# Kernel tuning notes

Hardware: AMD Instinct MI355X
Metric: run time of the kernel (lower is better)

## Reference

```python
import jax, jax.numpy as jnp
import numpy as np

B, T, D, U = 64, 2048, 256, 256
EPS = 1e-6


def setup_inputs() -> dict:
    key = jax.random.key(0)
    ks = jax.random.split(key, 4)
    x = jax.random.normal(ks[0], (B, T, D), dtype=jnp.float32)
    # glorot-ish scaled init for stability
    kernel = jax.random.normal(ks[1], (D, 3 * U), dtype=jnp.float32) * (1.0 / np.sqrt(D))
    rec_kernel = jax.random.normal(ks[2], (U, 3 * U), dtype=jnp.float32) * (1.0 / np.sqrt(U))
    bias = jnp.zeros((3 * U,), dtype=jnp.float32)
    ln_gamma = jnp.ones((U,), dtype=jnp.float32)
    ln_beta = jnp.zeros((U,), dtype=jnp.float32)
    return {"x": x, "kernel": kernel, "rec_kernel": rec_kernel, "bias": bias,
            "ln_gamma": ln_gamma, "ln_beta": ln_beta}


def _custom_gru(x, kernel, rec_kernel, bias):
    # Precompute input projection for all timesteps: [B,T,3U]
    xw = jnp.einsum('btd,dk->btk', x, kernel) + bias
    xw_t = jnp.swapaxes(xw, 0, 1)  # [T,B,3U] for scan
    h0 = jnp.zeros((x.shape[0], U), dtype=x.dtype)

    def step(h, xw_step):
        gates = xw_step + h @ rec_kernel            # [B,3U]
        z, r, h_hat_pre = jnp.split(gates, 3, axis=1)
        z = jax.nn.sigmoid(z)
        r = jax.nn.sigmoid(r)
        # nonstandard blend inside tanh (faithful to CustomGRUCell)
        h_hat = jnp.tanh(r * h_hat_pre + (1.0 - r) * h)
        h_new = (1.0 - z) * h_hat + z * h
        return h_new, h_new

    _, hs = jax.lax.scan(step, h0, xw_t)            # hs: [T,B,U]
    return jnp.swapaxes(hs, 0, 1)                   # [B,T,U]


def _layernorm(x, gamma, beta):
    mu = jnp.mean(x, axis=-1, keepdims=True)
    var = jnp.mean(jnp.square(x - mu), axis=-1, keepdims=True)
    return (x - mu) * jax.lax.rsqrt(var + EPS) * gamma + beta


def reference(x, kernel, rec_kernel, bias, ln_gamma, ln_beta):
    # call() returns only the GRU-stack branch (n=1 layer) + shared LayerNorm;
    # the embedded_inputs branch in the source is dead code.
    seq = _custom_gru(x, kernel, rec_kernel, bias)
    return _layernorm(seq, ln_gamma, ln_beta)
```

## Files before the change

### kernel.cpp

```cpp
#include <hip/hip_runtime.h>
#include <hip/hip_bf16.h>
#include <hip/hip_fp16.h>

using half4_t = __attribute__((ext_vector_type(4))) _Float16;
using half8_t = __attribute__((ext_vector_type(8))) _Float16;
using f32x4   = __attribute__((ext_vector_type(4))) float;
using i32x4   = __attribute__((ext_vector_type(4))) int;

#define B_   64
#define T_   2048
#define D_   256
#define U_   256
#define NG   768
#define TC   512
#define NCHUNK (T_/TC)
#define GB   16

typedef const __attribute__((address_space(1))) void* gptr_t;
typedef __attribute__((address_space(3))) void* lptr_t;

__device__ __forceinline__ float rcpf(float x) { return __builtin_amdgcn_rcpf(x); }


__global__ void conv_x_chunk(const float* __restrict__ x, _Float16* __restrict__ xh, int t0) {
  size_t idx = ((size_t)blockIdx.x * 256 + threadIdx.x) * 8;
  int b   = (int)(idx >> 17);
  int rem = (int)(idx & 131071);
  const float4* p = (const float4*)(x + ((size_t)(b * T_ + t0)) * D_ + rem);
  float4 v0 = p[0], v1 = p[1];
  half8_t o;
  o[0] = (_Float16)v0.x; o[1] = (_Float16)v0.y; o[2] = (_Float16)v0.z; o[3] = (_Float16)v0.w;
  o[4] = (_Float16)v1.x; o[5] = (_Float16)v1.y; o[6] = (_Float16)v1.z; o[7] = (_Float16)v1.w;
  *(half8_t*)(xh + idx) = o;
}

__global__ void conv_T(const float* __restrict__ src, _Float16* __restrict__ dst) {
  int idx = blockIdx.x * 256 + threadIdx.x;
  int d = idx / NG;
  int j = idx - d * NG;
  dst[j * 256 + d] = (_Float16)src[idx];
}


__global__ void init_scale(unsigned* s) { if (threadIdx.x == 0) *s = 0u; }

__global__ void absmax_rec(const float* __restrict__ rec, unsigned* __restrict__ s) {
  int i = (blockIdx.x * 256 + threadIdx.x) * 4;
  float4 v = *(const float4*)(rec + i);
  float m = fmaxf(fmaxf(fabsf(v.x), fabsf(v.y)), fmaxf(fabsf(v.z), fabsf(v.w)));
  #pragma unroll
  for (int off = 32; off >= 1; off >>= 1) m = fmaxf(m, __shfl_xor(m, off));
  __shared__ float sm[4];
  int l = threadIdx.x & 63, wv = threadIdx.x >> 6;
  if (l == 0) sm[wv] = m;
  __syncthreads();
  if (threadIdx.x == 0) {
    m = fmaxf(fmaxf(sm[0], sm[1]), fmaxf(sm[2], sm[3]));
    atomicMax(s, __float_as_uint(m));
  }
}

__global__ void conv_rec_i8(const float* __restrict__ rec, const unsigned* __restrict__ sc,
                            char* __restrict__ dst) {
  int idx = blockIdx.x * 256 + threadIdx.x;
  int j = idx & 15, l = (idx >> 4) & 63, sl = idx >> 10;
  int mt = sl >> 2, ks = sl & 3, bi = l & 15, hi = l >> 4;
  float am = __uint_as_float(*sc) + 1e-30f;
  float s = 127.f / am;
  float v = rec[(size_t)(ks * 64 + hi * 16 + j) * NG + mt * 16 + bi] * s;
  int q = __float2int_rn(v);
  q = q > 127 ? 127 : (q < -127 ? -127 : q);
  dst[idx] = (char)q;
}

#define BM 128
#define BN 128

__global__ __launch_bounds__(256, 2) void gemm16(
    const _Float16* __restrict__ A,
    const _Float16* __restrict__ BT,
    const float* __restrict__ bias,
    _Float16* __restrict__ xwl)
{
  __shared__ alignas(16) _Float16 As[BM * 32];
  __shared__ alignas(16) _Float16 Bs[BN * 32];
  const int tid = threadIdx.x, l = tid & 63, w = tid >> 6;
  const int NT = NG / BN;
  const int mt = blockIdx.x / NT, nt = blockIdx.x % NT;
  const char* Ab = (const char*)A  + (size_t)mt * BM * 512;
  const char* Bb = (const char*)BT + (size_t)nt * BN * 512;
  const int wm = (w & 1) * 64, wn = (w >> 1) * 64;
  f32x4 acc[4][4] = {};

  for (int kt = 0; kt < 8; ++kt) {
    #pragma unroll
    for (int s = 0; s < 2; ++s) {
      int c = tid + s * 256;
      int row = c >> 2, gq = c & 3;
      int gs = gq ^ ((row >> 1) & 3);
      __builtin_amdgcn_global_load_lds(
        (gptr_t)(Ab + (size_t)row * 512 + kt * 64 + gs * 16),
        (lptr_t)((char*)As + c * 16), 16, 0, 0);
    }
    #pragma unroll
    for (int s = 0; s < 2; ++s) {
      int c = tid + s * 256;
      int row = c >> 2, gq = c & 3;
      int gs = gq ^ ((row >> 1) & 3);
      __builtin_amdgcn_global_load_lds(
        (gptr_t)(Bb + (size_t)row * 512 + kt * 64 + gs * 16),
        (lptr_t)((char*)Bs + c * 16), 16, 0, 0);
    }
    __syncthreads();

    half8_t av[4], bv[4];
    #pragma unroll
    for (int m = 0; m < 4; ++m) {
      int row = wm + m * 16 + (l & 15);
      int off = row * 64 + (((l >> 4) ^ ((row >> 1) & 3)) << 4);
      av[m] = *(const half8_t*)((const char*)As + off);
    }
    #pragma unroll
    for (int n = 0; n < 4; ++n) {
      int row = wn + n * 16 + (l & 15);
      int off = row * 64 + (((l >> 4) ^ ((row >> 1) & 3)) << 4);
      bv[n] = *(const half8_t*)((const char*)Bs + off);
    }
    #pragma unroll
    for (int m = 0; m < 4; ++m)
      #pragma unroll
      for (int n = 0; n < 4; ++n)
        acc[m][n] = __builtin_amdgcn_mfma_f32_16x16x32_f16(av[m], bv[n], acc[m][n], 0, 0, 0);
    __syncthreads();
  }

  int m0 = mt * BM, n0 = nt * BN;
  #pragma unroll
  for (int m = 0; m < 4; ++m) {
    #pragma unroll
    for (int n = 0; n < 4; ++n) {
      int c = n0 + wn + n * 16 + (l & 15);
      int gate = c >> 8, uu = c & 255;
      int wv = uu >> 4, hq = (uu >> 2) & 3, qv = uu & 3;
      int lane_tid = wv * 64 + (qv << 2) + (hq << 4);
      float bc = bias[c];
      #pragma unroll
      for (int q = 0; q < 4; ++q) {
        int arow = m0 + wm + m * 16 + ((l >> 4) * 4 + q);
        int b = arow >> 9, tloc = arow & 511;
        int g = b >> 2, bidx = b & 3;
        size_t dst = ((size_t)(g * 512 + tloc) * 3 + gate) * 1024 + lane_tid + bidx;
        xwl[dst] = (_Float16)(acc[m][n][q] + bc);
      }
    }
  }
}


__global__ __launch_bounds__(1024) void scan_i8(
    const char* __restrict__ rq,
    const _Float16* __restrict__ xws,
    const unsigned* __restrict__ sc,
    float* __restrict__ out,
    float* __restrict__ hg,
    int t0)
{
  const int g = blockIdx.x, tid = threadIdx.x;
  const int w = tid >> 6, l = tid & 63, bi = l & 15, hi = l >> 4;
  const int bc = bi & 3, qq = bi >> 2;
  const int u = w * 16 + hi * 4 + qq;

  __shared__ alignas(16) char Hq[2][1024];

  const i32x4* rp = (const i32x4*)rq;
#define FR(mt, ks) rp[((mt) * 4 + (ks)) * 64 + l]
  i32x4 Az0 = FR(w, 0),      Az1 = FR(w, 1),      Az2 = FR(w, 2),      Az3 = FR(w, 3);
  i32x4 Ar0 = FR(16 + w, 0), Ar1 = FR(16 + w, 1), Ar2 = FR(16 + w, 2), Ar3 = FR(16 + w, 3);
  i32x4 Ah0 = FR(32 + w, 0), Ah1 = FR(32 + w, 1), Ah2 = FR(32 + w, 2), Ah3 = FR(32 + w, 3);
#undef FR
  asm volatile("" : "+v"(Az0), "+v"(Az1), "+v"(Az2), "+v"(Az3),
                    "+v"(Ar0), "+v"(Ar1), "+v"(Ar2), "+v"(Ar3),
                    "+v"(Ah0), "+v"(Ah1), "+v"(Ah2), "+v"(Ah3));

  const float dq = (__uint_as_float(*sc) + 1e-30f) / (127.f * 127.f);

  float h = (t0 == 0) ? 0.f : hg[(size_t)(g * 4 + bc) * 256 + u];

  const int hwa = bc * 256 + ((w ^ bc) << 4) + hi * 4 + qq;
  { int q8 = __float2int_rn(h * 127.f); Hq[0][hwa] = (char)q8; }

  const _Float16* xp = xws + (size_t)g * 512 * 3072 + tid;
  float* outp = out + ((size_t)(g * 4 + bc) * T_ + t0) * U_ + u;

  _Float16 nz = xp[0], nr = xp[1024], nh = xp[2048];
  __syncthreads();

  for (int t = 0; t < TC; ++t) {
    float xzf = (float)nz, xrf = (float)nr, xhf = (float)nh;
    {
      int tn = (t + 1 < TC) ? (t + 1) : t;
      const _Float16* xq = xp + (size_t)tn * 3072;
      nz = xq[0]; nr = xq[1024]; nh = xq[2048];
    }

    const char* hb = &Hq[t & 1][0];
    i32x4 az = {}, ar = {}, ah = {};
#define BADDR(ks) (bc * 256 + ((((ks) * 4 + hi) ^ bc) << 4))
    { i32x4 Bf;
      Bf = *(const i32x4*)(hb + BADDR(0));
      az = __builtin_amdgcn_mfma_i32_16x16x64_i8(Az0, Bf, az, 0, 0, 0);
      ar = __builtin_amdgcn_mfma_i32_16x16x64_i8(Ar0, Bf, ar, 0, 0, 0);
      ah = __builtin_amdgcn_mfma_i32_16x16x64_i8(Ah0, Bf, ah, 0, 0, 0);
      Bf = *(const i32x4*)(hb + BADDR(1));
      az = __builtin_amdgcn_mfma_i32_16x16x64_i8(Az1, Bf, az, 0, 0, 0);
      ar = __builtin_amdgcn_mfma_i32_16x16x64_i8(Ar1, Bf, ar, 0, 0, 0);
      ah = __builtin_amdgcn_mfma_i32_16x16x64_i8(Ah1, Bf, ah, 0, 0, 0);
      Bf = *(const i32x4*)(hb + BADDR(2));
      az = __builtin_amdgcn_mfma_i32_16x16x64_i8(Az2, Bf, az, 0, 0, 0);
      ar = __builtin_amdgcn_mfma_i32_16x16x64_i8(Ar2, Bf, ar, 0, 0, 0);
      ah = __builtin_amdgcn_mfma_i32_16x16x64_i8(Ah2, Bf, ah, 0, 0, 0);
      Bf = *(const i32x4*)(hb + BADDR(3));
      az = __builtin_amdgcn_mfma_i32_16x16x64_i8(Az3, Bf, az, 0, 0, 0);
      ar = __builtin_amdgcn_mfma_i32_16x16x64_i8(Ar3, Bf, ar, 0, 0, 0);
      ah = __builtin_amdgcn_mfma_i32_16x16x64_i8(Ah3, Bf, ah, 0, 0, 0);
    }
#undef BADDR

#define SEL4(a) ((qq & 2) ? ((qq & 1) ? (a)[3] : (a)[2]) : ((qq & 1) ? (a)[1] : (a)[0]))
    float pz = (float)SEL4(az) * dq + xzf;
    float pr = (float)SEL4(ar) * dq + xrf;
    float ph = (float)SEL4(ah) * dq + xhf;
#undef SEL4
    float z  = rcpf(1.f + __expf(-pz));
    float r  = rcpf(1.f + __expf(-pr));
    float y  = r * (ph - h) + h;
    float th = 2.f * rcpf(1.f + __expf(-2.f * y)) - 1.f;
    h = z * (h - th) + th;

    outp[(size_t)t * U_] = h;
    int q8 = __float2int_rn(h * 127.f);
    Hq[(t & 1) ^ 1][hwa] = (char)q8;
    __syncthreads();
  }

  hg[(size_t)(g * 4 + bc) * 256 + u] = h;
}

__global__ __launch_bounds__(256) void ln_rows(
    float* __restrict__ io,
    const float* __restrict__ gamma, const float* __restrict__ beta, int t0)
{
  int rid = blockIdx.x * 4 + (threadIdx.x >> 6);
  int l = threadIdx.x & 63;
  int b = rid >> 9, tl = rid & 511;
  float* p = io + ((size_t)b * T_ + t0 + tl) * U_ + l * 4;
  f32x4 v = *(const f32x4*)p;
  float s  = (v[0] + v[1]) + (v[2] + v[3]);
  float s2 = (v[0]*v[0] + v[1]*v[1]) + (v[2]*v[2] + v[3]*v[3]);
  #pragma unroll
  for (int off = 1; off <= 32; off <<= 1) {
    s  += __shfl_xor(s, off);
    s2 += __shfl_xor(s2, off);
  }
  float mu = s * (1.f / 256.f);
  float var = s2 * (1.f / 256.f) - mu * mu;
  float rs = rsqrtf(var + 1e-6f);
  f32x4 gm = *(const f32x4*)(gamma + l * 4);
  f32x4 bt = *(const f32x4*)(beta + l * 4);
  f32x4 o;
  o[0] = (v[0] - mu) * rs * gm[0] + bt[0];
  o[1] = (v[1] - mu) * rs * gm[1] + bt[1];
  o[2] = (v[2] - mu) * rs * gm[2] + bt[2];
  o[3] = (v[3] - mu) * rs * gm[3] + bt[3];
  *(f32x4*)p = o;
}

extern "C" void kernel_launch(void* const* d_in, const int* in_sizes, int n_in,
                              void* d_out, int out_size, void* d_ws, size_t ws_size,
                              hipStream_t stream) {
  const float* x     = (const float*)d_in[0];
  const float* kern  = (const float*)d_in[1];
  const float* rec   = (const float*)d_in[2];
  const float* bias  = (const float*)d_in[3];
  const float* gamma = (const float*)d_in[4];
  const float* beta  = (const float*)d_in[5];
  float* out = (float*)d_out;
  char* ws = (char*)d_ws;

  _Float16* xws = (_Float16*)(ws);
  _Float16* xhc = (_Float16*)(ws + 50331648);
  _Float16* kT  = (_Float16*)(ws + 67108864);
  char*     rq  = (char*)    (ws + 67502080);
  unsigned* sc  = (unsigned*)(ws + 67698688);
  float*    hg  = (float*)   (ws + 67698720);

  init_scale<<<1, 64, 0, stream>>>(sc);
  absmax_rec<<<192, 256, 0, stream>>>(rec, sc);
  conv_T<<<768, 256, 0, stream>>>(kern, kT);
  conv_rec_i8<<<768, 256, 0, stream>>>(rec, sc, rq);

  for (int c = 0; c < NCHUNK; ++c) {
    int t0 = c * TC;
    conv_x_chunk<<<4096, 256, 0, stream>>>(x, xhc, t0);
    gemm16<<<(B_ * TC / BM) * (NG / BN), 256, 0, stream>>>(xhc, kT, bias, xws);
    scan_i8<<<GB, 1024, 0, stream>>>(rq, xws, sc, out, hg, t0);
    ln_rows<<<(B_ * TC) / 4, 256, 0, stream>>>(out, gamma, beta, t0);
  }
}
```

Before: 1.581 ms.

## Fuse scan, GEMM and LayerNorm into one kernel and pipeline chunks

Replaces the separate gemm16, scan_i8 and ln_rows kernels with one 'mega' kernel that dispatches on block index to scan, GEMM-tile or LayerNorm work. The host schedule is software-pipelined over time chunks: the 16 latency-bound scan blocks for chunk c run alongside the GEMM for chunk c+1 and the LayerNorm for chunk c-1, using double-buffered projection buffers. This aims to hide input-projection and normalization time behind the sequential recurrence and to fill idle CUs. The projection layout now interleaves z and r gates as half2, so the scan loads them in one access. Risks: the pipelined path only runs when the workspace is large enough, and co-running blocks may contend with the scan for memory bandwidth.

```diff
diff --git a/kernel.cpp b/kernel.cpp
--- a/kernel.cpp
+++ b/kernel.cpp
@@ -2,7 +2,7 @@
 #include <hip/hip_bf16.h>
 #include <hip/hip_fp16.h>
 
-using half4_t = __attribute__((ext_vector_type(4))) _Float16;
+using half2_t = __attribute__((ext_vector_type(2))) _Float16;
 using half8_t = __attribute__((ext_vector_type(8))) _Float16;
 using f32x4   = __attribute__((ext_vector_type(4))) float;
 using i32x4   = __attribute__((ext_vector_type(4))) int;
@@ -14,7 +14,9 @@
 #define NG   768
 #define TC   512
 #define NCHUNK (T_/TC)
-#define GB   16
+#define GB_SCAN 16
+#define GB_GEMM 1536
+#define GB_LN   2048
 
 typedef const __attribute__((address_space(1))) void* gptr_t;
 typedef __attribute__((address_space(3))) void* lptr_t;
@@ -40,7 +42,6 @@
   int j = idx - d * NG;
   dst[j * 256 + d] = (_Float16)src[idx];
 }
-
 
 __global__ void init_scale(unsigned* s) { if (threadIdx.x == 0) *s = 0u; }
 
@@ -73,206 +74,209 @@
   dst[idx] = (char)q;
 }
 
-#define BM 128
-#define BN 128
-
-__global__ __launch_bounds__(256, 2) void gemm16(
-    const _Float16* __restrict__ A,
-    const _Float16* __restrict__ BT,
-    const float* __restrict__ bias,
-    _Float16* __restrict__ xwl)
-{
-  __shared__ alignas(16) _Float16 As[BM * 32];
-  __shared__ alignas(16) _Float16 Bs[BN * 32];
-  const int tid = threadIdx.x, l = tid & 63, w = tid >> 6;
-  const int NT = NG / BN;
-  const int mt = blockIdx.x / NT, nt = blockIdx.x % NT;
-  const char* Ab = (const char*)A  + (size_t)mt * BM * 512;
-  const char* Bb = (const char*)BT + (size_t)nt * BN * 512;
-  const int wm = (w & 1) * 64, wn = (w >> 1) * 64;
-  f32x4 acc[4][4] = {};
-
-  for (int kt = 0; kt < 8; ++kt) {
-    #pragma unroll
-    for (int s = 0; s < 2; ++s) {
-      int c = tid + s * 256;
-      int row = c >> 2, gq = c & 3;
-      int gs = gq ^ ((row >> 1) & 3);
-      __builtin_amdgcn_global_load_lds(
-        (gptr_t)(Ab + (size_t)row * 512 + kt * 64 + gs * 16),
-        (lptr_t)((char*)As + c * 16), 16, 0, 0);
-    }
-    #pragma unroll
-    for (int s = 0; s < 2; ++s) {
-      int c = tid + s * 256;
-      int row = c >> 2, gq = c & 3;
-      int gs = gq ^ ((row >> 1) & 3);
-      __builtin_amdgcn_global_load_lds(
-        (gptr_t)(Bb + (size_t)row * 512 + kt * 64 + gs * 16),
-        (lptr_t)((char*)Bs + c * 16), 16, 0, 0);
-    }
-    __syncthreads();
-
-    half8_t av[4], bv[4];
-    #pragma unroll
-    for (int m = 0; m < 4; ++m) {
-      int row = wm + m * 16 + (l & 15);
-      int off = row * 64 + (((l >> 4) ^ ((row >> 1) & 3)) << 4);
-      av[m] = *(const half8_t*)((const char*)As + off);
-    }
-    #pragma unroll
-    for (int n = 0; n < 4; ++n) {
-      int row = wn + n * 16 + (l & 15);
-      int off = row * 64 + (((l >> 4) ^ ((row >> 1) & 3)) << 4);
-      bv[n] = *(const half8_t*)((const char*)Bs + off);
-    }
-    #pragma unroll
-    for (int m = 0; m < 4; ++m)
-      #pragma unroll
-      for (int n = 0; n < 4; ++n)
-        acc[m][n] = __builtin_amdgcn_mfma_f32_16x16x32_f16(av[m], bv[n], acc[m][n], 0, 0, 0);
-    __syncthreads();
-  }
-
-  int m0 = mt * BM, n0 = nt * BN;
-  #pragma unroll
-  for (int m = 0; m < 4; ++m) {
-    #pragma unroll
-    for (int n = 0; n < 4; ++n) {
-      int c = n0 + wn + n * 16 + (l & 15);
-      int gate = c >> 8, uu = c & 255;
-      int wv = uu >> 4, hq = (uu >> 2) & 3, qv = uu & 3;
-      int lane_tid = wv * 64 + (qv << 2) + (hq << 4);
-      float bc = bias[c];
-      #pragma unroll
-      for (int q = 0; q < 4; ++q) {
-        int arow = m0 + wm + m * 16 + ((l >> 4) * 4 + q);
-        int b = arow >> 9, tloc = arow & 511;
-        int g = b >> 2, bidx = b & 3;
-        size_t dst = ((size_t)(g * 512 + tloc) * 3 + gate) * 1024 + lane_tid + bidx;
-        xwl[dst] = (_Float16)(acc[m][n][q] + bc);
-      }
-    }
-  }
-}
-
-
-__global__ __launch_bounds__(1024) void scan_i8(
+
+__global__ __launch_bounds__(1024) void mega(
     const char* __restrict__ rq,
-    const _Float16* __restrict__ xws,
+    const _Float16* __restrict__ xwsS,
     const unsigned* __restrict__ sc,
     float* __restrict__ out,
     float* __restrict__ hg,
-    int t0)
+    int scanT0,
+    const _Float16* __restrict__ xhc,
+    const _Float16* __restrict__ kT,
+    const float* __restrict__ bias,
+    _Float16* __restrict__ xwsG,
+    const float* __restrict__ gamma,
+    const float* __restrict__ beta,
+    int lnT0,
+    int nScan, int nGemm)
 {
-  const int g = blockIdx.x, tid = threadIdx.x;
-  const int w = tid >> 6, l = tid & 63, bi = l & 15, hi = l >> 4;
-  const int bc = bi & 3, qq = bi >> 2;
-  const int u = w * 16 + hi * 4 + qq;
-
-  __shared__ alignas(16) char Hq[2][1024];
-
-  const i32x4* rp = (const i32x4*)rq;
+  __shared__ union UU {
+    struct { char Hq[2][1024]; } s;
+    struct { alignas(16) _Float16 As[128 * 32]; alignas(16) _Float16 Bs[128 * 32]; } g;
+  } U;
+
+  int bid = blockIdx.x;
+  const int tid = threadIdx.x;
+
+  if (bid < nScan) {
+    const int g = bid;
+    const int w = tid >> 6, l = tid & 63, bi = l & 15, hi = l >> 4;
+    const int bc = bi & 3, qq = bi >> 2;
+    const int u = w * 16 + hi * 4 + qq;
+
+    const i32x4* rp = (const i32x4*)rq;
 #define FR(mt, ks) rp[((mt) * 4 + (ks)) * 64 + l]
-  i32x4 Az0 = FR(w, 0),      Az1 = FR(w, 1),      Az2 = FR(w, 2),      Az3 = FR(w, 3);
-  i32x4 Ar0 = FR(16 + w, 0), Ar1 = FR(16 + w, 1), Ar2 = FR(16 + w, 2), Ar3 = FR(16 + w, 3);
-  i32x4 Ah0 = FR(32 + w, 0), Ah1 = FR(32 + w, 1), Ah2 = FR(32 + w, 2), Ah3 = FR(32 + w, 3);
+    i32x4 Az0 = FR(w, 0),      Az1 = FR(w, 1),      Az2 = FR(w, 2),      Az3 = FR(w, 3);
+    i32x4 Ar0 = FR(16 + w, 0), Ar1 = FR(16 + w, 1), Ar2 = FR(16 + w, 2), Ar3 = FR(16 + w, 3);
+    i32x4 Ah0 = FR(32 + w, 0), Ah1 = FR(32 + w, 1), Ah2 = FR(32 + w, 2), Ah3 = FR(32 + w, 3);
 #undef FR
-  asm volatile("" : "+v"(Az0), "+v"(Az1), "+v"(Az2), "+v"(Az3),
-                    "+v"(Ar0), "+v"(Ar1), "+v"(Ar2), "+v"(Ar3),
-                    "+v"(Ah0), "+v"(Ah1), "+v"(Ah2), "+v"(Ah3));
-
-  const float dq = (__uint_as_float(*sc) + 1e-30f) / (127.f * 127.f);
-
-  float h = (t0 == 0) ? 0.f : hg[(size_t)(g * 4 + bc) * 256 + u];
-
-  const int hwa = bc * 256 + ((w ^ bc) << 4) + hi * 4 + qq;
-  { int q8 = __float2int_rn(h * 127.f); Hq[0][hwa] = (char)q8; }
-
-  const _Float16* xp = xws + (size_t)g * 512 * 3072 + tid;
-  float* outp = out + ((size_t)(g * 4 + bc) * T_ + t0) * U_ + u;
-
-  _Float16 nz = xp[0], nr = xp[1024], nh = xp[2048];
-  __syncthreads();
-
-  for (int t = 0; t < TC; ++t) {
-    float xzf = (float)nz, xrf = (float)nr, xhf = (float)nh;
-    {
-      int tn = (t + 1 < TC) ? (t + 1) : t;
-      const _Float16* xq = xp + (size_t)tn * 3072;
-      nz = xq[0]; nr = xq[1024]; nh = xq[2048];
-    }
-
-    const char* hb = &Hq[t & 1][0];
-    i32x4 az = {}, ar = {}, ah = {};
+    asm volatile("" : "+v"(Az0), "+v"(Az1), "+v"(Az2), "+v"(Az3),
+                      "+v"(Ar0), "+v"(Ar1), "+v"(Ar2), "+v"(Ar3),
+                      "+v"(Ah0), "+v"(Ah1), "+v"(Ah2), "+v"(Ah3));
+
+    const float dq = (__uint_as_float(*sc) + 1e-30f) / (127.f * 127.f);
+
+    float h = (scanT0 == 0) ? 0.f : hg[(size_t)(g * 4 + bc) * 256 + u];
+
+    const int hwa = bc * 256 + ((w ^ bc) << 4) + hi * 4 + qq;
+    { int q8 = __float2int_rn(h * 127.f); U.s.Hq[0][hwa] = (char)q8; }
+
+    const char* xpg = (const char*)xwsS + (size_t)g * TC * 6144;
+    float* outp = out + ((size_t)(g * 4 + bc) * T_ + scanT0) * U_ + u;
+
+    unsigned nzr = *(const unsigned*)(xpg + tid * 4);
+    _Float16 nh2 = *(const _Float16*)(xpg + 4096 + tid * 2);
+    __syncthreads();
+
+    for (int t = 0; t < TC; ++t) {
+      half2_t zrp = __builtin_bit_cast(half2_t, nzr);
+      float xzf = (float)zrp[0], xrf = (float)zrp[1], xhf = (float)nh2;
+      {
+        int tn = (t + 1 < TC) ? (t + 1) : t;
+        nzr = *(const unsigned*)(xpg + (size_t)tn * 6144 + tid * 4);
+        nh2 = *(const _Float16*)(xpg + (size_t)tn * 6144 + 4096 + tid * 2);
+      }
+
+      const char* hb = &U.s.Hq[t & 1][0];
+      i32x4 az = {}, ar = {}, ah = {};
 #define BADDR(ks) (bc * 256 + ((((ks) * 4 + hi) ^ bc) << 4))
-    { i32x4 Bf;
-      Bf = *(const i32x4*)(hb + BADDR(0));
-      az = __builtin_amdgcn_mfma_i32_16x16x64_i8(Az0, Bf, az, 0, 0, 0);
-      ar = __builtin_amdgcn_mfma_i32_16x16x64_i8(Ar0, Bf, ar, 0, 0, 0);
-      ah = __builtin_amdgcn_mfma_i32_16x16x64_i8(Ah0, Bf, ah, 0, 0, 0);
-      Bf = *(const i32x4*)(hb + BADDR(1));
-      az = __builtin_amdgcn_mfma_i32_16x16x64_i8(Az1, Bf, az, 0, 0, 0);
-      ar = __builtin_amdgcn_mfma_i32_16x16x64_i8(Ar1, Bf, ar, 0, 0, 0);
-      ah = __builtin_amdgcn_mfma_i32_16x16x64_i8(Ah1, Bf, ah, 0, 0, 0);
-      Bf = *(const i32x4*)(hb + BADDR(2));
-      az = __builtin_amdgcn_mfma_i32_16x16x64_i8(Az2, Bf, az, 0, 0, 0);
-      ar = __builtin_amdgcn_mfma_i32_16x16x64_i8(Ar2, Bf, ar, 0, 0, 0);
-      ah = __builtin_amdgcn_mfma_i32_16x16x64_i8(Ah2, Bf, ah, 0, 0, 0);
-      Bf = *(const i32x4*)(hb + BADDR(3));
-      az = __builtin_amdgcn_mfma_i32_16x16x64_i8(Az3, Bf, az, 0, 0, 0);
-      ar = __builtin_amdgcn_mfma_i32_16x16x64_i8(Ar3, Bf, ar, 0, 0, 0);
-      ah = __builtin_amdgcn_mfma_i32_16x16x64_i8(Ah3, Bf, ah, 0, 0, 0);
-    }
+      { i32x4 Bf;
+        Bf = *(const i32x4*)(hb + BADDR(0));
+        az = __builtin_amdgcn_mfma_i32_16x16x64_i8(Az0, Bf, az, 0, 0, 0);
+        ar = __builtin_amdgcn_mfma_i32_16x16x64_i8(Ar0, Bf, ar, 0, 0, 0);
+        ah = __builtin_amdgcn_mfma_i32_16x16x64_i8(Ah0, Bf, ah, 0, 0, 0);
+        Bf = *(const i32x4*)(hb + BADDR(1));
+        az = __builtin_amdgcn_mfma_i32_16x16x64_i8(Az1, Bf, az, 0, 0, 0);
+        ar = __builtin_amdgcn_mfma_i32_16x16x64_i8(Ar1, Bf, ar, 0, 0, 0);
+        ah = __builtin_amdgcn_mfma_i32_16x16x64_i8(Ah1, Bf, ah, 0, 0, 0);
+        Bf = *(const i32x4*)(hb + BADDR(2));
+        az = __builtin_amdgcn_mfma_i32_16x16x64_i8(Az2, Bf, az, 0, 0, 0);
+        ar = __builtin_amdgcn_mfma_i32_16x16x64_i8(Ar2, Bf, ar, 0, 0, 0);
+        ah = __builtin_amdgcn_mfma_i32_16x16x64_i8(Ah2, Bf, ah, 0, 0, 0);
+        Bf = *(const i32x4*)(hb + BADDR(3));
+        az = __builtin_amdgcn_mfma_i32_16x16x64_i8(Az3, Bf, az, 0, 0, 0);
+        ar = __builtin_amdgcn_mfma_i32_16x16x64_i8(Ar3, Bf, ar, 0, 0, 0);
+        ah = __builtin_amdgcn_mfma_i32_16x16x64_i8(Ah3, Bf, ah, 0, 0, 0);
+      }
 #undef BADDR
 
 #define SEL4(a) ((qq & 2) ? ((qq & 1) ? (a)[3] : (a)[2]) : ((qq & 1) ? (a)[1] : (a)[0]))
-    float pz = (float)SEL4(az) * dq + xzf;
-    float pr = (float)SEL4(ar) * dq + xrf;
-    float ph = (float)SEL4(ah) * dq + xhf;
+      float pz = (float)SEL4(az) * dq + xzf;
+      float pr = (float)SEL4(ar) * dq + xrf;
+      float ph = (float)SEL4(ah) * dq + xhf;
 #undef SEL4
-    float z  = rcpf(1.f + __expf(-pz));
-    float r  = rcpf(1.f + __expf(-pr));
-    float y  = r * (ph - h) + h;
-    float th = 2.f * rcpf(1.f + __expf(-2.f * y)) - 1.f;
-    h = z * (h - th) + th;
-
-    outp[(size_t)t * U_] = h;
-    int q8 = __float2int_rn(h * 127.f);
-    Hq[(t & 1) ^ 1][hwa] = (char)q8;
-    __syncthreads();
-  }
-
-  hg[(size_t)(g * 4 + bc) * 256 + u] = h;
-}
-
-__global__ __launch_bounds__(256) void ln_rows(
-    float* __restrict__ io,
-    const float* __restrict__ gamma, const float* __restrict__ beta, int t0)
-{
-  int rid = blockIdx.x * 4 + (threadIdx.x >> 6);
-  int l = threadIdx.x & 63;
-  int b = rid >> 9, tl = rid & 511;
-  float* p = io + ((size_t)b * T_ + t0 + tl) * U_ + l * 4;
-  f32x4 v = *(const f32x4*)p;
-  float s  = (v[0] + v[1]) + (v[2] + v[3]);
-  float s2 = (v[0]*v[0] + v[1]*v[1]) + (v[2]*v[2] + v[3]*v[3]);
-  #pragma unroll
-  for (int off = 1; off <= 32; off <<= 1) {
-    s  += __shfl_xor(s, off);
-    s2 += __shfl_xor(s2, off);
-  }
-  float mu = s * (1.f / 256.f);
-  float var = s2 * (1.f / 256.f) - mu * mu;
-  float rs = rsqrtf(var + 1e-6f);
-  f32x4 gm = *(const f32x4*)(gamma + l * 4);
-  f32x4 bt = *(const f32x4*)(beta + l * 4);
-  f32x4 o;
-  o[0] = (v[0] - mu) * rs * gm[0] + bt[0];
-  o[1] = (v[1] - mu) * rs * gm[1] + bt[1];
-  o[2] = (v[2] - mu) * rs * gm[2] + bt[2];
-  o[3] = (v[3] - mu) * rs * gm[3] + bt[3];
-  *(f32x4*)p = o;
+      float z  = rcpf(1.f + __expf(-pz));
+      float r  = rcpf(1.f + __expf(-pr));
+      float y  = r * (ph - h) + h;
+      float th = 2.f * rcpf(1.f + __expf(-2.f * y)) - 1.f;
+      h = z * (h - th) + th;
+
+      outp[(size_t)t * U_] = h;
+      int q8 = __float2int_rn(h * 127.f);
+      U.s.Hq[(t & 1) ^ 1][hwa] = (char)q8;
+      __syncthreads();
+    }
+
+    hg[(size_t)(g * 4 + bc) * 256 + u] = h;
+    return;
+  }
+  bid -= nScan;
+
+  if (bid < nGemm) {
+    const int tile = bid;
+    const int mt = tile / 6, nt = tile % 6;
+    const int w = tid >> 6, l = tid & 63;
+    const int wm = (w & 3) * 32, wn = (w >> 2) * 32;
+    const char* Ab = (const char*)xhc + (size_t)mt * 128 * 512;
+    const char* Bb = (const char*)kT  + (size_t)nt * 128 * 512;
+    f32x4 acc[2][2] = {};
+
+    const bool isA = tid < 512;
+    const int cc = isA ? tid : tid - 512;
+    const int srow = cc >> 2, sgq = cc & 3;
+    const int sgs = sgq ^ ((srow >> 1) & 3);
+    const char* sb = isA ? Ab : Bb;
+    char* ldsb = (char*)(isA ? U.g.As : U.g.Bs) + cc * 16;
+
+    for (int kt = 0; kt < 8; ++kt) {
+      __builtin_amdgcn_global_load_lds(
+        (gptr_t)(sb + (size_t)srow * 512 + kt * 64 + sgs * 16),
+        (lptr_t)ldsb, 16, 0, 0);
+      __syncthreads();
+
+      half8_t av[2], bv[2];
+      #pragma unroll
+      for (int mi = 0; mi < 2; ++mi) {
+        int row = wm + mi * 16 + (l & 15);
+        int off = row * 64 + (((l >> 4) ^ ((row >> 1) & 3)) << 4);
+        av[mi] = *(const half8_t*)((const char*)U.g.As + off);
+      }
+      #pragma unroll
+      for (int ni = 0; ni < 2; ++ni) {
+        int row = wn + ni * 16 + (l & 15);
+        int off = row * 64 + (((l >> 4) ^ ((row >> 1) & 3)) << 4);
+        bv[ni] = *(const half8_t*)((const char*)U.g.Bs + off);
+      }
+      #pragma unroll
+      for (int mi = 0; mi < 2; ++mi)
+        #pragma unroll
+        for (int ni = 0; ni < 2; ++ni)
+          acc[mi][ni] = __builtin_amdgcn_mfma_f32_16x16x32_f16(av[mi], bv[ni], acc[mi][ni], 0, 0, 0);
+      __syncthreads();
+    }
+
+    #pragma unroll
+    for (int mi = 0; mi < 2; ++mi) {
+      #pragma unroll
+      for (int ni = 0; ni < 2; ++ni) {
+        int c = nt * 128 + wn + ni * 16 + (l & 15);
+        int cgate = c >> 8, uu = c & 255;
+        int wv = uu >> 4, hq = (uu >> 2) & 3, qv = uu & 3;
+        int lane_tid = wv * 64 + (qv << 2) + (hq << 4);
+        float bc = bias[c];
+        #pragma unroll
+        for (int q = 0; q < 4; ++q) {
+          int arow = mt * 128 + wm + mi * 16 + ((l >> 4) * 4 + q);
+          int b = arow >> 9, tloc = arow & 511;
+          int g = b >> 2, bidx = b & 3;
+          int lane = lane_tid + bidx;
+          size_t page = (size_t)(g * 512 + tloc) * 3072;
+          size_t dst = (cgate < 2) ? (page + (size_t)lane * 2 + cgate)
+                                   : (page + 2048 + lane);
+          xwsG[dst] = (_Float16)(acc[mi][ni][q] + bc);
+        }
+      }
+    }
+    return;
+  }
+  bid -= nGemm;
+
+  {
+    int rid = bid * 16 + (tid >> 6);
+    int l = tid & 63;
+    int b = rid >> 9, tl = rid & 511;
+    float* p = out + ((size_t)b * T_ + lnT0 + tl) * U_ + l * 4;
+    f32x4 v = *(const f32x4*)p;
+    float s  = (v[0] + v[1]) + (v[2] + v[3]);
+    float s2 = (v[0]*v[0] + v[1]*v[1]) + (v[2]*v[2] + v[3]*v[3]);
+    #pragma unroll
+    for (int off = 1; off <= 32; off <<= 1) {
+      s  += __shfl_xor(s, off);
+      s2 += __shfl_xor(s2, off);
+    }
+    float mu = s * (1.f / 256.f);
+    float var = s2 * (1.f / 256.f) - mu * mu;
+    float rs = rsqrtf(var + 1e-6f);
+    f32x4 gm = *(const f32x4*)(gamma + l * 4);
+    f32x4 bt = *(const f32x4*)(beta + l * 4);
+    f32x4 o;
+    o[0] = (v[0] - mu) * rs * gm[0] + bt[0];
+    o[1] = (v[1] - mu) * rs * gm[1] + bt[1];
+    o[2] = (v[2] - mu) * rs * gm[2] + bt[2];
+    o[3] = (v[3] - mu) * rs * gm[3] + bt[3];
+    *(f32x4*)p = o;
+  }
 }
 
 extern "C" void kernel_launch(void* const* d_in, const int* in_sizes, int n_in,
@@ -287,23 +291,61 @@
   float* out = (float*)d_out;
   char* ws = (char*)d_ws;
 
-  _Float16* xws = (_Float16*)(ws);
-  _Float16* xhc = (_Float16*)(ws + 50331648);
-  _Float16* kT  = (_Float16*)(ws + 67108864);
-  char*     rq  = (char*)    (ws + 67502080);
-  unsigned* sc  = (unsigned*)(ws + 67698688);
-  float*    hg  = (float*)   (ws + 67698720);
+  const size_t XWS = 50331648;
+  const bool pipe = (ws_size >= 118096000ull);
+
+  _Float16* xwsA = (_Float16*)ws;
+  _Float16* xwsB = pipe ? (_Float16*)(ws + XWS) : xwsA;
+  size_t o = pipe ? 2 * XWS : XWS;
+  _Float16* xhc = (_Float16*)(ws + o);           o += 16777216;
+  _Float16* kT  = (_Float16*)(ws + o);           o += 393216;
+  char*     rq  = (char*)    (ws + o);           o += 196608;
+  unsigned* sc  = (unsigned*)(ws + o);           o += 128;
+  float*    hg  = (float*)   (ws + o);
 
   init_scale<<<1, 64, 0, stream>>>(sc);
   absmax_rec<<<192, 256, 0, stream>>>(rec, sc);
   conv_T<<<768, 256, 0, stream>>>(kern, kT);
   conv_rec_i8<<<768, 256, 0, stream>>>(rec, sc, rq);
 
-  for (int c = 0; c < NCHUNK; ++c) {
-    int t0 = c * TC;
-    conv_x_chunk<<<4096, 256, 0, stream>>>(x, xhc, t0);
-    gemm16<<<(B_ * TC / BM) * (NG / BN), 256, 0, stream>>>(xhc, kT, bias, xws);
-    scan_i8<<<GB, 1024, 0, stream>>>(rq, xws, sc, out, hg, t0);
-    ln_rows<<<(B_ * TC) / 4, 256, 0, stream>>>(out, gamma, beta, t0);
-  }
-}
+  if (pipe) {
+    _Float16* xb[2] = { xwsA, xwsB };
+    conv_x_chunk<<<4096, 256, 0, stream>>>(x, xhc, 0);
+    mega<<<GB_GEMM, 1024, 0, stream>>>(rq, xwsA, sc, out, hg, 0,
+                                       xhc, kT, bias, xwsA, gamma, beta, 0,
+                                       0, GB_GEMM);
+    conv_x_chunk<<<4096, 256, 0, stream>>>(x, xhc, TC);
+    mega<<<GB_SCAN + GB_GEMM, 1024, 0, stream>>>(rq, xwsA, sc, out, hg, 0,
+                                       xhc, kT, bias, xwsB, gamma, beta, 0,
+                                       GB_SCAN, GB_GEMM);
+    conv_x_chunk<<<4096, 256, 0, stream>>>(x, xhc, 2 * TC);
+    mega<<<GB_SCAN + GB_GEMM + GB_LN, 1024, 0, stream>>>(rq, xwsB, sc, out, hg, TC,
+                                       xhc, kT, bias, xwsA, gamma, beta, 0,
+                                       GB_SCAN, GB_GEMM);
+    conv_x_chunk<<<4096, 256, 0, stream>>>(x, xhc, 3 * TC);
+    mega<<<GB_SCAN + GB_GEMM + GB_LN, 1024, 0, stream>>>(rq, xwsA, sc, out, hg, 2 * TC,
+                                       xhc, kT, bias, xwsB, gamma, beta, TC,
+                                       GB_SCAN, GB_GEMM);
+    mega<<<GB_SCAN + GB_LN, 1024, 0, stream>>>(rq, xwsB, sc, out, hg, 3 * TC,
+                                       xhc, kT, bias, xwsA, gamma, beta, 2 * TC,
+                                       GB_SCAN, 0);
+    mega<<<GB_LN, 1024, 0, stream>>>(rq, xwsA, sc, out, hg, 0,
+                                       xhc, kT, bias, xwsA, gamma, beta, 3 * TC,
+                                       0, 0);
+    (void)xb;
+  } else {
+    for (int c = 0; c < NCHUNK; ++c) {
+      int t0 = c * TC;
+      conv_x_chunk<<<4096, 256, 0, stream>>>(x, xhc, t0);
+      mega<<<GB_GEMM, 1024, 0, stream>>>(rq, xwsA, sc, out, hg, t0,
+                                         xhc, kT, bias, xwsA, gamma, beta, t0,
+                                         0, GB_GEMM);
+      mega<<<GB_SCAN, 1024, 0, stream>>>(rq, xwsA, sc, out, hg, t0,
+                                         xhc, kT, bias, xwsA, gamma, beta, t0,
+                                         GB_SCAN, 0);
+      mega<<<GB_LN, 1024, 0, stream>>>(rq, xwsA, sc, out, hg, t0,
+                                       xhc, kT, bias, xwsA, gamma, beta, t0,
+                                       0, 0);
+    }
+  }
+}
```

New measurement: 1.466 ms. -7.3%, faster.
